# Performance work log

Hardware: AMD Instinct MI355X
Metric: run time of the kernel (lower is better)

## Reference

```python
import jax, jax.numpy as jnp
import numpy as np

D_MODEL = 1024
N_HEADS = 16
N_KV_HEADS = 4
HEAD_DIM = D_MODEL // N_HEADS  # 64
N_REP = N_HEADS // N_KV_HEADS  # 4
THETA = 10000.0
LOGIT_CAP = 30.0
EPS = 1e-6
SCALE = HEAD_DIM ** -0.5


def rmsnorm(x, w):
    return x * jax.lax.rsqrt(jnp.mean(x * x, axis=-1, keepdims=True) + EPS) * w


def rope_tables(seq_len, dtype):
    inv_freq = 1.0 / (THETA ** (jnp.arange(0, HEAD_DIM, 2, dtype=jnp.float32) / HEAD_DIM))
    t = jnp.arange(seq_len, dtype=jnp.float32)
    freqs = jnp.outer(t, inv_freq)                      # [S, hd/2]
    emb = jnp.concatenate([freqs, freqs], axis=-1)      # [S, hd]
    return jnp.cos(emb).astype(dtype), jnp.sin(emb).astype(dtype)


def rotate_half(x):
    x1, x2 = jnp.split(x, 2, axis=-1)
    return jnp.concatenate([-x2, x1], axis=-1)


def apply_rope(x, cos, sin):
    # x: [B, H, S, hd]; cos/sin: [S, hd] broadcast over (B, H)
    return x * cos + rotate_half(x) * sin


def setup_inputs() -> dict:
    key = jax.random.key(0)
    ks = jax.random.split(key, 7)
    B, S = 4, 2048
    w = 0.02
    return {
        "x": jax.random.normal(ks[0], (B, S, D_MODEL), dtype=jnp.float32),
        "Wq": jax.random.normal(ks[1], (N_HEADS * HEAD_DIM, D_MODEL), dtype=jnp.float32) * w,
        "Wk": jax.random.normal(ks[2], (N_KV_HEADS * HEAD_DIM, D_MODEL), dtype=jnp.float32) * w,
        "Wv": jax.random.normal(ks[3], (N_KV_HEADS * HEAD_DIM, D_MODEL), dtype=jnp.float32) * w,
        "Wo": jax.random.normal(ks[4], (D_MODEL, N_HEADS * HEAD_DIM), dtype=jnp.float32) * w,
        "q_norm_w": jnp.ones((HEAD_DIM,), dtype=jnp.float32),
        "k_norm_w": jnp.ones((HEAD_DIM,), dtype=jnp.float32),
    }


def reference(x, Wq, Wk, Wv, Wo, q_norm_w, k_norm_w):
    B, S, _ = x.shape
    # projections (nn.Linear: y = x @ W^T)
    q = (x @ Wq.T).reshape(B, S, N_HEADS, HEAD_DIM).transpose(0, 2, 1, 3)      # [B,H,S,d]
    k = (x @ Wk.T).reshape(B, S, N_KV_HEADS, HEAD_DIM).transpose(0, 2, 1, 3)   # [B,Hkv,S,d]
    v = (x @ Wv.T).reshape(B, S, N_KV_HEADS, HEAD_DIM).transpose(0, 2, 1, 3)
    # QK-RMSNorm
    q = rmsnorm(q, q_norm_w)
    k = rmsnorm(k, k_norm_w)
    # RoPE
    cos, sin = rope_tables(S, x.dtype)
    q = apply_rope(q, cos, sin)
    k = apply_rope(k, cos, sin)
    # GQA expand (repeat_interleave over head dim)
    k_exp = jnp.repeat(k, N_REP, axis=1)  # [B,H,S,d]
    v_exp = jnp.repeat(v, N_REP, axis=1)
    # soft-capped attention (training path)
    scores = jnp.einsum('bhqd,bhkd->bhqk', q, k_exp) * SCALE
    scores = LOGIT_CAP * jnp.tanh(scores / LOGIT_CAP)
    causal = jnp.triu(jnp.ones((S, S), dtype=bool), k=1)  # kv_len - seq_len + 1 = 1
    scores = jnp.where(causal, -jnp.inf, scores)
    attn = jax.nn.softmax(scores, axis=-1)
    out = jnp.einsum('bhqk,bhkd->bhqd', attn, v_exp)
    out = out.transpose(0, 2, 1, 3).reshape(B, S, N_HEADS * HEAD_DIM)
    return out @ Wo.T
```

## Files before the change

### kernel.cpp

```cpp
#include <hip/hip_runtime.h>
#include <hip/hip_bf16.h>
#include <math.h>
#include <stdint.h>

#define D_MODEL 1024
#define NHEADS  16
#define NKV     4
#define HD      64
#define SEQ     2048
#define BATCH   4
#define MTOK    (BATCH*SEQ)
#define NQKV    (D_MODEL + 2*NKV*HD)
#define ASCALE  0.125f
#define CAP     30.0f

using f32x4  = __attribute__((ext_vector_type(4))) float;
using bf16x8 = __attribute__((ext_vector_type(8))) short;

__device__ __forceinline__ unsigned short f2bf(float f) {
  union { float f; unsigned u; } v; v.f = f;
  unsigned u = v.u + 0x7fffu + ((v.u >> 16) & 1u);
  return (unsigned short)(u >> 16);
}
__device__ __forceinline__ unsigned short f2bf_hup(float f) {
  union { float f; unsigned u; } v; v.f = f;
  return (unsigned short)((v.u + 0x8000u) >> 16);
}
__device__ __forceinline__ void async_copy16(void* lds, const void* g) {
  __builtin_amdgcn_global_load_lds(
      (const __attribute__((address_space(1))) unsigned int*)(uintptr_t)g,
      (__attribute__((address_space(3))) unsigned int*)(uintptr_t)lds, 16, 0, 0);
}

__global__ __launch_bounds__(256) void cvt_all(
    const float* __restrict__ x, const float* __restrict__ wq,
    const float* __restrict__ wk, const float* __restrict__ wv,
    const float* __restrict__ wo,
    unsigned short* __restrict__ xb, unsigned short* __restrict__ wqkv,
    unsigned short* __restrict__ wob) {
  const long i = (long)(blockIdx.x * 256 + threadIdx.x) * 4;
  const float* src; unsigned short* dst; long off;
  if (i < 8388608L)      { src = x;  dst = xb;             off = i; }
  else if (i < 9437184L) { src = wq; dst = wqkv;           off = i - 8388608L; }
  else if (i < 9699328L) { src = wk; dst = wqkv + 1048576; off = i - 9437184L; }
  else if (i < 9961472L) { src = wv; dst = wqkv + 1310720; off = i - 9699328L; }
  else                   { src = wo; dst = wob;            off = i - 9961472L; }
  float4 v = *(const float4*)(src + off);
  ushort4 o; o.x = f2bf(v.x); o.y = f2bf(v.y); o.z = f2bf(v.z); o.w = f2bf(v.w);
  *(ushort4*)(dst + off) = o;
}

__global__ __launch_bounds__(256) void gemm_qkv(
    const unsigned short* __restrict__ A, const unsigned short* __restrict__ B,
    const float* __restrict__ qw, const float* __restrict__ kw,
    unsigned short* __restrict__ Qn, unsigned short* __restrict__ Kn,
    unsigned short* __restrict__ Vt) {
  __shared__ __align__(16) unsigned short As[128 * 32];
  __shared__ __align__(16) unsigned short Bs[128 * 32];
  const int t = threadIdx.x;
  const int w = t >> 6, l = t & 63;
  const int mb = blockIdx.x, nb = blockIdx.y;
  const int wm = w & 1, wn = w >> 1;
  const int quad = l >> 4, ln = l & 15;
  const int K = D_MODEL;
  f32x4 acc[4][4] = {};
  const unsigned short* Ag = A + (size_t)(mb * 128 + w * 32) * K;
  const unsigned short* Bg = B + (size_t)(nb * 128 + w * 32) * K;
  char* Asw = (char*)As + w * 2048;
  char* Bsw = (char*)Bs + w * 2048;
  const int lrow = l >> 2, lcol = (l & 3) * 8;

  for (int kb = 0; kb < K; kb += 32) {
    async_copy16(Asw + l * 16,        Ag + (size_t)lrow * K + kb + lcol);
    async_copy16(Asw + 1024 + l * 16, Ag + (size_t)(16 + lrow) * K + kb + lcol);
    async_copy16(Bsw + l * 16,        Bg + (size_t)lrow * K + kb + lcol);
    async_copy16(Bsw + 1024 + l * 16, Bg + (size_t)(16 + lrow) * K + kb + lcol);
    __syncthreads();
    bf16x8 af[4], bfr[4];
#pragma unroll
    for (int mt = 0; mt < 4; ++mt)
      af[mt] = *(const bf16x8*)(As + (wm * 64 + mt * 16 + ln) * 32 + quad * 8);
#pragma unroll
    for (int nt = 0; nt < 4; ++nt)
      bfr[nt] = *(const bf16x8*)(Bs + (wn * 64 + nt * 16 + ln) * 32 + quad * 8);
#pragma unroll
    for (int mt = 0; mt < 4; ++mt)
#pragma unroll
      for (int nt = 0; nt < 4; ++nt)
        acc[mt][nt] = __builtin_amdgcn_mfma_f32_16x16x32_bf16(af[mt], bfr[nt], acc[mt][nt], 0, 0, 0);
    __syncthreads();
  }

  const int hs = nb * 2 + wn;
  const int bB = mb >> 4;
  const int sBase = ((mb & 15) * 128) + wm * 64;

  if (hs < 20) {
    const float* wgt = (hs < 16) ? qw : kw;
    float wv_[4];
#pragma unroll
    for (int nt = 0; nt < 4; ++nt) wv_[nt] = wgt[nt * 16 + ln];
    const float f0 = __expf(-(float)ln * 0.2878231366f);
    const float f1 = f0 * 0.01f;
    unsigned short* dst = (hs < 16)
        ? Qn + (size_t)(bB * 16 + hs) * SEQ * 64
        : Kn + (size_t)(bB * 4 + (hs - 16)) * SEQ * 64;
#pragma unroll
    for (int mt = 0; mt < 4; ++mt) {
#pragma unroll
      for (int r = 0; r < 4; ++r) {
        const int sTok = sBase + mt * 16 + quad * 4 + r;
        float ss = 0.f;
#pragma unroll
        for (int nt = 0; nt < 4; ++nt) ss = fmaf(acc[mt][nt][r], acc[mt][nt][r], ss);
        ss += __shfl_xor(ss, 1, 64); ss += __shfl_xor(ss, 2, 64);
        ss += __shfl_xor(ss, 4, 64); ss += __shfl_xor(ss, 8, 64);
        const float inv = rsqrtf(ss * (1.0f / 64.0f) + 1e-6f);
        float xn[4];
#pragma unroll
        for (int nt = 0; nt < 4; ++nt) xn[nt] = acc[mt][nt][r] * inv * wv_[nt];
        float sn0, cs0, sn1, cs1;
        __sincosf((float)sTok * f0, &sn0, &cs0);
        __sincosf((float)sTok * f1, &sn1, &cs1);
        const float o0 = xn[0] * cs0 - xn[2] * sn0;
        const float o1 = xn[1] * cs1 - xn[3] * sn1;
        const float o2 = xn[2] * cs0 + xn[0] * sn0;
        const float o3 = xn[3] * cs1 + xn[1] * sn1;
        const size_t ro = (size_t)sTok * 64 + ln;
        dst[ro]      = f2bf(o0);
        dst[ro + 16] = f2bf(o1);
        dst[ro + 32] = f2bf(o2);
        dst[ro + 48] = f2bf(o3);
      }
    }
  } else {
    unsigned short* dst = Vt + (size_t)(bB * 4 + (hs - 20)) * 64 * SEQ;
#pragma unroll
    for (int mt = 0; mt < 4; ++mt)
#pragma unroll
      for (int nt = 0; nt < 4; ++nt)
#pragma unroll
        for (int r = 0; r < 4; ++r) {
          const int sTok = sBase + mt * 16 + quad * 4 + r;
          dst[(size_t)(nt * 16 + ln) * SEQ + sTok] = f2bf(acc[mt][nt][r]);
        }
  }
}

__global__ __launch_bounds__(256) void gemm_bt_f32(
    const unsigned short* __restrict__ A, const unsigned short* __restrict__ B,
    float* __restrict__ C, int M, int N, int K) {
  __shared__ __align__(16) unsigned short As[128 * 32];
  __shared__ __align__(16) unsigned short Bs[128 * 32];
  const int t = threadIdx.x;
  const int w = t >> 6, l = t & 63;
  const int mb = blockIdx.x, nb = blockIdx.y;
  const int wm = w & 1, wn = w >> 1;
  f32x4 acc[4][4] = {};
  const unsigned short* Ag = A + (size_t)(mb * 128 + w * 32) * K;
  const unsigned short* Bg = B + (size_t)(nb * 128 + w * 32) * K;
  char* Asw = (char*)As + w * 2048;
  char* Bsw = (char*)Bs + w * 2048;
  const int lrow = l >> 2, lcol = (l & 3) * 8;

  for (int kb = 0; kb < K; kb += 32) {
    async_copy16(Asw + l * 16,        Ag + (size_t)lrow * K + kb + lcol);
    async_copy16(Asw + 1024 + l * 16, Ag + (size_t)(16 + lrow) * K + kb + lcol);
    async_copy16(Bsw + l * 16,        Bg + (size_t)lrow * K + kb + lcol);
    async_copy16(Bsw + 1024 + l * 16, Bg + (size_t)(16 + lrow) * K + kb + lcol);
    __syncthreads();
    bf16x8 af[4], bfr[4];
#pragma unroll
    for (int mt = 0; mt < 4; ++mt)
      af[mt] = *(const bf16x8*)(As + (wm * 64 + mt * 16 + (l & 15)) * 32 + (l >> 4) * 8);
#pragma unroll
    for (int nt = 0; nt < 4; ++nt)
      bfr[nt] = *(const bf16x8*)(Bs + (wn * 64 + nt * 16 + (l & 15)) * 32 + (l >> 4) * 8);
#pragma unroll
    for (int mt = 0; mt < 4; ++mt)
#pragma unroll
      for (int nt = 0; nt < 4; ++nt)
        acc[mt][nt] = __builtin_amdgcn_mfma_f32_16x16x32_bf16(af[mt], bfr[nt], acc[mt][nt], 0, 0, 0);
    __syncthreads();
  }
  const int row0 = mb * 128 + wm * 64, col0 = nb * 128 + wn * 64;
#pragma unroll
  for (int mt = 0; mt < 4; ++mt)
#pragma unroll
    for (int nt = 0; nt < 4; ++nt)
#pragma unroll
      for (int r = 0; r < 4; ++r) {
        int row = row0 + mt * 16 + (l >> 4) * 4 + r;
        int col = col0 + nt * 16 + (l & 15);
        C[(size_t)row * N + col] = acc[mt][nt][r];
      }
}

template<bool DIAG>
__device__ __forceinline__ void attn_tile(
    const unsigned short* __restrict__ Kg, const unsigned short* __restrict__ Vg,
    int kv0, const bf16x8* aq, f32x4* o_acc, float* l_part,
    unsigned short* Ks, unsigned short* Vs, unsigned short* Ps,
    int w, int l, int quad, int ln, int lrow, int lc) {
  __syncthreads();
#pragma unroll
  for (int i = 0; i < 2; ++i) {
    int s = w * 2 + i;
    int snt = s >> 1, sks = s & 1;
    async_copy16((char*)Ks + s * 1024,
                 Kg + (size_t)(kv0 + snt * 16 + lrow) * 64 + sks * 32 + lc);
    async_copy16((char*)Vs + s * 1024,
                 Vg + (size_t)(snt * 16 + lrow) * SEQ + kv0 + sks * 32 + lc);
  }
  __syncthreads();

  f32x4 sacc[4] = {};
#pragma unroll
  for (int nt = 0; nt < 4; ++nt)
#pragma unroll
    for (int ks = 0; ks < 2; ++ks) {
      bf16x8 bk = *(const bf16x8*)((char*)Ks + (nt * 2 + ks) * 1024 + ln * 64 + quad * 16);
      sacc[nt] = __builtin_amdgcn_mfma_f32_16x16x32_bf16(aq[ks], bk, sacc[nt], 0, 0, 0);
    }

  const float C  = 0.18033688011112042f;
  const float B1 = -5.787037037e-6f;
  const float B2 = 4.0187757201e-11f;
  const float M2 = 11.541560327f;
#pragma unroll
  for (int nt = 0; nt < 4; ++nt) {
    const int col = nt * 16 + ln;
    const int base = w * 1024 + (col >> 5) * 512 + ((((col >> 3) & 3) ^ quad) << 3) + (col & 7);
#pragma unroll
    for (int r = 0; r < 4; ++r) {
      float s = sacc[nt][r];
      float s2 = s * s;
      float tt = fmaf(s2, B2, B1);
      tt = fmaf(s2, tt, 1.0f);
      float pr = exp2f(fmaf(s * C, tt, -M2));
      if (DIAG && col > (w * 16 + quad * 4 + r)) pr = 0.0f;
      l_part[r] += pr;
      Ps[base + (quad * 4 + r) * 32] = f2bf_hup(pr);
    }
  }
  __builtin_amdgcn_s_waitcnt(0xc07f);

  bf16x8 ap[2];
#pragma unroll
  for (int ks = 0; ks < 2; ++ks)
    ap[ks] = *(const bf16x8*)((char*)Ps + w * 2048 + ks * 1024 + ln * 64 +
                              ((quad ^ (ln >> 2)) << 4));
#pragma unroll
  for (int nt = 0; nt < 4; ++nt)
#pragma unroll
    for (int ks = 0; ks < 2; ++ks) {
      bf16x8 bv = *(const bf16x8*)((char*)Vs + (nt * 2 + ks) * 1024 + ln * 64 + quad * 16);
      o_acc[nt] = __builtin_amdgcn_mfma_f32_16x16x32_bf16(ap[ks], bv, o_acc[nt], 0, 0, 0);
    }
}

__global__ __launch_bounds__(256) void attn(
    const unsigned short* __restrict__ Qn, const unsigned short* __restrict__ Kn,
    const unsigned short* __restrict__ Vtg, unsigned short* __restrict__ O) {
  __shared__ __align__(16) unsigned short Ks[4096];
  __shared__ __align__(16) unsigned short Vs[4096];
  __shared__ __align__(16) unsigned short Ps[4096];
  const int t = threadIdx.x, w = t >> 6, l = t & 63;
  const int quad = l >> 4, ln = l & 15;
  const int qt = 31 - (int)(blockIdx.x >> 6);
  const int bh = blockIdx.x & 63;
  const int h = bh & 15, b = bh >> 4;
  const int q0 = qt * 64;
  const unsigned short* Qh = Qn + ((size_t)(b * 16 + h)) * SEQ * 64;
  const unsigned short* Kg = Kn + ((size_t)(b * 4 + (h >> 2))) * SEQ * 64;
  const unsigned short* Vg = Vtg + ((size_t)(b * 4 + (h >> 2))) * 64 * SEQ;
  const int lrow = l >> 2, lc = (l & 3) * 8;

  bf16x8 aq[2];
#pragma unroll
  for (int ks = 0; ks < 2; ++ks)
    aq[ks] = *(const bf16x8*)(Qh + (size_t)(q0 + w * 16 + ln) * 64 + ks * 32 + quad * 8);
  f32x4 o_acc[4] = {};
  float l_part[4] = {0.f, 0.f, 0.f, 0.f};

  for (int j = 0; j < qt; ++j)
    attn_tile<false>(Kg, Vg, j * 64, aq, o_acc, l_part, Ks, Vs, Ps, w, l, quad, ln, lrow, lc);
  attn_tile<true>(Kg, Vg, qt * 64, aq, o_acc, l_part, Ks, Vs, Ps, w, l, quad, ln, lrow, lc);

  float invl[4];
#pragma unroll
  for (int r = 0; r < 4; ++r) {
    float s = l_part[r];
    s += __shfl_xor(s, 1, 64); s += __shfl_xor(s, 2, 64);
    s += __shfl_xor(s, 4, 64); s += __shfl_xor(s, 8, 64);
    invl[r] = 1.0f / s;
  }
#pragma unroll
  for (int nt = 0; nt < 4; ++nt)
#pragma unroll
    for (int r = 0; r < 4; ++r) {
      int qrow = q0 + w * 16 + quad * 4 + r;
      int col = h * 64 + nt * 16 + ln;
      O[((size_t)(b * SEQ + qrow)) * 1024 + col] = f2bf_hup(o_acc[nt][r] * invl[r]);
    }
}

extern "C" void kernel_launch(void* const* d_in, const int* in_sizes, int n_in,
                              void* d_out, int out_size, void* d_ws, size_t ws_size,
                              hipStream_t stream) {
  const float* x  = (const float*)d_in[0];
  const float* Wq = (const float*)d_in[1];
  const float* Wk = (const float*)d_in[2];
  const float* Wv = (const float*)d_in[3];
  const float* Wo = (const float*)d_in[4];
  const float* qw = (const float*)d_in[5];
  const float* kw = (const float*)d_in[6];
  float* out = (float*)d_out;

  char* ws = (char*)d_ws;
  unsigned short* xb   = (unsigned short*)(ws);
  unsigned short* wqkv = (unsigned short*)(ws + 16777216);
  unsigned short* wo   = (unsigned short*)(ws + 19922944);
  unsigned short* Qn   = (unsigned short*)(ws + 22020096);
  unsigned short* Kn   = (unsigned short*)(ws + 38797312);
  unsigned short* Vtg  = (unsigned short*)(ws + 42991616);
  unsigned short* Ob   = (unsigned short*)(ws + 47185920);

  cvt_all<<<10752, 256, 0, stream>>>(x, Wq, Wk, Wv, Wo, xb, wqkv, wo);
  gemm_qkv<<<dim3(MTOK / 128, NQKV / 128), 256, 0, stream>>>(xb, wqkv, qw, kw, Qn, Kn, Vtg);
  attn<<<2048, 256, 0, stream>>>(Qn, Kn, Vtg, Ob);
  gemm_bt_f32<<<dim3(MTOK / 128, 1024 / 128), 256, 0, stream>>>(Ob, wo, out, MTOK, 1024, 1024);
}
```

Before: 253.0 us.

## Enlarge attention query tile to 128 rows per block and balance causal work

Each attention block now handles 128 query rows instead of 64, with every wave computing two 16-row m-tiles. This reuses each K/V tile loaded into LDS across twice as many queries, halving K/V traffic and block count. A new block-index mapping pairs long and short causal rows so work stays balanced, and waves whose rows lie wholly before a KV tile skip compute for it. It also switches to hardware exp2 and rcp intrinsics and adds an occupancy hint, at the cost of more registers, twice the P scratch in LDS, and idle waves during diagonal tiles.

```diff
diff --git a/kernel.cpp b/kernel.cpp
--- a/kernel.cpp
+++ b/kernel.cpp
@@ -25,6 +25,9 @@
 __device__ __forceinline__ unsigned short f2bf_hup(float f) {
   union { float f; unsigned u; } v; v.f = f;
   return (unsigned short)((v.u + 0x8000u) >> 16);
+}
+__device__ __forceinline__ float fexp2(float x) {
+  return __builtin_amdgcn_exp2f(x);
 }
 __device__ __forceinline__ void async_copy16(void* lds, const void* g) {
   __builtin_amdgcn_global_load_lds(
@@ -196,113 +199,125 @@
       }
 }
 
-template<bool DIAG>
-__device__ __forceinline__ void attn_tile(
-    const unsigned short* __restrict__ Kg, const unsigned short* __restrict__ Vg,
-    int kv0, const bf16x8* aq, f32x4* o_acc, float* l_part,
-    unsigned short* Ks, unsigned short* Vs, unsigned short* Ps,
-    int w, int l, int quad, int ln, int lrow, int lc) {
-  __syncthreads();
-#pragma unroll
-  for (int i = 0; i < 2; ++i) {
-    int s = w * 2 + i;
-    int snt = s >> 1, sks = s & 1;
-    async_copy16((char*)Ks + s * 1024,
-                 Kg + (size_t)(kv0 + snt * 16 + lrow) * 64 + sks * 32 + lc);
-    async_copy16((char*)Vs + s * 1024,
-                 Vg + (size_t)(snt * 16 + lrow) * SEQ + kv0 + sks * 32 + lc);
-  }
-  __syncthreads();
-
-  f32x4 sacc[4] = {};
-#pragma unroll
-  for (int nt = 0; nt < 4; ++nt)
-#pragma unroll
-    for (int ks = 0; ks < 2; ++ks) {
-      bf16x8 bk = *(const bf16x8*)((char*)Ks + (nt * 2 + ks) * 1024 + ln * 64 + quad * 16);
-      sacc[nt] = __builtin_amdgcn_mfma_f32_16x16x32_bf16(aq[ks], bk, sacc[nt], 0, 0, 0);
-    }
-
-  const float C  = 0.18033688011112042f;
-  const float B1 = -5.787037037e-6f;
-  const float B2 = 4.0187757201e-11f;
-  const float M2 = 11.541560327f;
-#pragma unroll
-  for (int nt = 0; nt < 4; ++nt) {
-    const int col = nt * 16 + ln;
-    const int base = w * 1024 + (col >> 5) * 512 + ((((col >> 3) & 3) ^ quad) << 3) + (col & 7);
-#pragma unroll
-    for (int r = 0; r < 4; ++r) {
-      float s = sacc[nt][r];
-      float s2 = s * s;
-      float tt = fmaf(s2, B2, B1);
-      tt = fmaf(s2, tt, 1.0f);
-      float pr = exp2f(fmaf(s * C, tt, -M2));
-      if (DIAG && col > (w * 16 + quad * 4 + r)) pr = 0.0f;
-      l_part[r] += pr;
-      Ps[base + (quad * 4 + r) * 32] = f2bf_hup(pr);
-    }
-  }
-  __builtin_amdgcn_s_waitcnt(0xc07f);
-
-  bf16x8 ap[2];
-#pragma unroll
-  for (int ks = 0; ks < 2; ++ks)
-    ap[ks] = *(const bf16x8*)((char*)Ps + w * 2048 + ks * 1024 + ln * 64 +
-                              ((quad ^ (ln >> 2)) << 4));
-#pragma unroll
-  for (int nt = 0; nt < 4; ++nt)
-#pragma unroll
-    for (int ks = 0; ks < 2; ++ks) {
-      bf16x8 bv = *(const bf16x8*)((char*)Vs + (nt * 2 + ks) * 1024 + ln * 64 + quad * 16);
-      o_acc[nt] = __builtin_amdgcn_mfma_f32_16x16x32_bf16(ap[ks], bv, o_acc[nt], 0, 0, 0);
-    }
-}
-
-__global__ __launch_bounds__(256) void attn(
+__global__ __launch_bounds__(256, 4) void attn(
     const unsigned short* __restrict__ Qn, const unsigned short* __restrict__ Kn,
     const unsigned short* __restrict__ Vtg, unsigned short* __restrict__ O) {
   __shared__ __align__(16) unsigned short Ks[4096];
   __shared__ __align__(16) unsigned short Vs[4096];
-  __shared__ __align__(16) unsigned short Ps[4096];
+  __shared__ __align__(16) unsigned short Ps[8192];
   const int t = threadIdx.x, w = t >> 6, l = t & 63;
   const int quad = l >> 4, ln = l & 15;
-  const int qt = 31 - (int)(blockIdx.x >> 6);
-  const int bh = blockIdx.x & 63;
+  const int bid = blockIdx.x;
+  const int jsl = bid & 3, krd = bid >> 8;
+  const int qt = (krd & 1) ? (2 * jsl + (krd >> 1)) : (15 - 2 * jsl - (krd >> 1));
+  const int bh = (bid >> 2) & 63;
   const int h = bh & 15, b = bh >> 4;
-  const int q0 = qt * 64;
+  const int q0 = qt * 128;
+  const int wq0 = q0 + w * 32;
   const unsigned short* Qh = Qn + ((size_t)(b * 16 + h)) * SEQ * 64;
   const unsigned short* Kg = Kn + ((size_t)(b * 4 + (h >> 2))) * SEQ * 64;
   const unsigned short* Vg = Vtg + ((size_t)(b * 4 + (h >> 2))) * 64 * SEQ;
   const int lrow = l >> 2, lc = (l & 3) * 8;
 
-  bf16x8 aq[2];
-#pragma unroll
-  for (int ks = 0; ks < 2; ++ks)
-    aq[ks] = *(const bf16x8*)(Qh + (size_t)(q0 + w * 16 + ln) * 64 + ks * 32 + quad * 8);
-  f32x4 o_acc[4] = {};
-  float l_part[4] = {0.f, 0.f, 0.f, 0.f};
-
-  for (int j = 0; j < qt; ++j)
-    attn_tile<false>(Kg, Vg, j * 64, aq, o_acc, l_part, Ks, Vs, Ps, w, l, quad, ln, lrow, lc);
-  attn_tile<true>(Kg, Vg, qt * 64, aq, o_acc, l_part, Ks, Vs, Ps, w, l, quad, ln, lrow, lc);
-
-  float invl[4];
-#pragma unroll
-  for (int r = 0; r < 4; ++r) {
-    float s = l_part[r];
-    s += __shfl_xor(s, 1, 64); s += __shfl_xor(s, 2, 64);
-    s += __shfl_xor(s, 4, 64); s += __shfl_xor(s, 8, 64);
-    invl[r] = 1.0f / s;
+  bf16x8 aq[2][2];
+#pragma unroll
+  for (int mt = 0; mt < 2; ++mt)
+#pragma unroll
+    for (int ks = 0; ks < 2; ++ks)
+      aq[mt][ks] = *(const bf16x8*)(Qh + (size_t)(wq0 + mt * 16 + ln) * 64 + ks * 32 + quad * 8);
+  f32x4 o_acc[2][4] = {};
+  float l_part[2][4] = {};
+
+  const float Cc = 0.18033688011112042f;
+  const float B1 = -5.787037037e-6f;
+  const float B2 = 4.0187757201e-11f;
+  const float M2 = 11.541560327f;
+
+  const int jmax = 2 * qt + 2;
+  for (int jj = 0; jj < jmax; ++jj) {
+    const int kv0 = jj * 64;
+    __syncthreads();
+#pragma unroll
+    for (int i = 0; i < 2; ++i) {
+      int s = w * 2 + i;
+      int snt = s >> 1, sks = s & 1;
+      async_copy16((char*)Ks + s * 1024,
+                   Kg + (size_t)(kv0 + snt * 16 + lrow) * 64 + sks * 32 + lc);
+      async_copy16((char*)Vs + s * 1024,
+                   Vg + (size_t)(snt * 16 + lrow) * SEQ + kv0 + sks * 32 + lc);
+    }
+    __syncthreads();
+    if (kv0 > wq0 + 31) continue;
+
+    f32x4 sacc[2][4] = {};
+#pragma unroll
+    for (int nt = 0; nt < 4; ++nt)
+#pragma unroll
+      for (int ks = 0; ks < 2; ++ks) {
+        bf16x8 bk = *(const bf16x8*)((char*)Ks + (nt * 2 + ks) * 1024 + ln * 64 + quad * 16);
+        sacc[0][nt] = __builtin_amdgcn_mfma_f32_16x16x32_bf16(aq[0][ks], bk, sacc[0][nt], 0, 0, 0);
+        sacc[1][nt] = __builtin_amdgcn_mfma_f32_16x16x32_bf16(aq[1][ks], bk, sacc[1][nt], 0, 0, 0);
+      }
+
+    const bool needMask = (kv0 + 63 > wq0);
+#pragma unroll
+    for (int mt = 0; mt < 2; ++mt)
+#pragma unroll
+      for (int nt = 0; nt < 4; ++nt) {
+        const int col = nt * 16 + ln;
+        const int base = w * 2048 + mt * 1024 + (col >> 5) * 512 +
+                         ((((col >> 3) & 3) ^ quad) << 3) + (col & 7);
+#pragma unroll
+        for (int r = 0; r < 4; ++r) {
+          float s = sacc[mt][nt][r];
+          float s2 = s * s;
+          float tt = fmaf(s2, B2, B1);
+          tt = fmaf(s2, tt, 1.0f);
+          float pr = fexp2(fmaf(s * Cc, tt, -M2));
+          if (needMask && (kv0 + col) > (wq0 + mt * 16 + quad * 4 + r)) pr = 0.0f;
+          l_part[mt][r] += pr;
+          Ps[base + (quad * 4 + r) * 32] = f2bf_hup(pr);
+        }
+      }
+    __builtin_amdgcn_s_waitcnt(0xc07f);
+
+    bf16x8 ap[2][2];
+#pragma unroll
+    for (int mt = 0; mt < 2; ++mt)
+#pragma unroll
+      for (int ks = 0; ks < 2; ++ks)
+        ap[mt][ks] = *(const bf16x8*)((char*)Ps + w * 4096 + mt * 2048 + ks * 1024 +
+                                      ln * 64 + ((quad ^ (ln >> 2)) << 4));
+#pragma unroll
+    for (int nt = 0; nt < 4; ++nt)
+#pragma unroll
+      for (int ks = 0; ks < 2; ++ks) {
+        bf16x8 bv = *(const bf16x8*)((char*)Vs + (nt * 2 + ks) * 1024 + ln * 64 + quad * 16);
+        o_acc[0][nt] = __builtin_amdgcn_mfma_f32_16x16x32_bf16(ap[0][ks], bv, o_acc[0][nt], 0, 0, 0);
+        o_acc[1][nt] = __builtin_amdgcn_mfma_f32_16x16x32_bf16(ap[1][ks], bv, o_acc[1][nt], 0, 0, 0);
+      }
   }
-#pragma unroll
-  for (int nt = 0; nt < 4; ++nt)
+
+  float invl[2][4];
+#pragma unroll
+  for (int mt = 0; mt < 2; ++mt)
 #pragma unroll
     for (int r = 0; r < 4; ++r) {
-      int qrow = q0 + w * 16 + quad * 4 + r;
-      int col = h * 64 + nt * 16 + ln;
-      O[((size_t)(b * SEQ + qrow)) * 1024 + col] = f2bf_hup(o_acc[nt][r] * invl[r]);
+      float s = l_part[mt][r];
+      s += __shfl_xor(s, 1, 64); s += __shfl_xor(s, 2, 64);
+      s += __shfl_xor(s, 4, 64); s += __shfl_xor(s, 8, 64);
+      invl[mt][r] = __builtin_amdgcn_rcpf(s);
     }
+#pragma unroll
+  for (int mt = 0; mt < 2; ++mt)
+#pragma unroll
+    for (int nt = 0; nt < 4; ++nt)
+#pragma unroll
+      for (int r = 0; r < 4; ++r) {
+        int qrow = wq0 + mt * 16 + quad * 4 + r;
+        int col = h * 64 + nt * 16 + ln;
+        O[((size_t)(b * SEQ + qrow)) * 1024 + col] = f2bf_hup(o_acc[mt][nt][r] * invl[mt][r]);
+      }
 }
 
 extern "C" void kernel_launch(void* const* d_in, const int* in_sizes, int n_in,
@@ -328,6 +343,6 @@
 
   cvt_all<<<10752, 256, 0, stream>>>(x, Wq, Wk, Wv, Wo, xb, wqkv, wo);
   gemm_qkv<<<dim3(MTOK / 128, NQKV / 128), 256, 0, stream>>>(xb, wqkv, qw, kw, Qn, Kn, Vtg);
-  attn<<<2048, 256, 0, stream>>>(Qn, Kn, Vtg, Ob);
+  attn<<<1024, 256, 0, stream>>>(Qn, Kn, Vtg, Ob);
   gemm_bt_f32<<<dim3(MTOK / 128, 1024 / 128), 256, 0, stream>>>(Ob, wo, out, MTOK, 1024, 1024);
 }
```

Measured after the change: 250.5 us. Within noise of the previous version (-1.0%).
